# Performance work log

Measured on AMD Instinct MI355X. Metric: run time of the kernel, lower is better.

Reference implementation:

```python
import jax, jax.numpy as jnp
import numpy as np


def _bilinear_sample(img, x_s, y_s):
    # img: [B,H,W,C], x_s/y_s: [B,H,W] normalized coords in [-1,1]
    B, H, W, C = img.shape
    # map [-1,1] -> pixel coords [0, W-1] / [0, H-1]
    x = 0.5 * (x_s + 1.0) * (W - 1)
    y = 0.5 * (y_s + 1.0) * (H - 1)

    x0 = jnp.floor(x).astype(jnp.int32)
    x1 = x0 + 1
    y0 = jnp.floor(y).astype(jnp.int32)
    y1 = y0 + 1

    x0c = jnp.clip(x0, 0, W - 1)
    x1c = jnp.clip(x1, 0, W - 1)
    y0c = jnp.clip(y0, 0, H - 1)
    y1c = jnp.clip(y1, 0, H - 1)

    b = jnp.arange(B, dtype=jnp.int32)[:, None, None]  # [B,1,1] broadcast over H,W
    Ia = img[b, y0c, x0c]  # [B,H,W,C] top-left
    Ib = img[b, y1c, x0c]  # bottom-left
    Ic = img[b, y0c, x1c]  # top-right
    Id = img[b, y1c, x1c]  # bottom-right

    x0f = x0c.astype(img.dtype)
    x1f = x1c.astype(img.dtype)
    y0f = y0c.astype(img.dtype)
    y1f = y1c.astype(img.dtype)

    wa = ((x1f - x) * (y1f - y))[..., None]
    wb = ((x1f - x) * (y - y0f))[..., None]
    wc = ((x - x0f) * (y1f - y))[..., None]
    wd = ((x - x0f) * (y - y0f))[..., None]

    return wa * Ia + wb * Ib + wc * Ic + wd * Id


def setup_inputs() -> dict:
    key = jax.random.key(0)
    k1, k2, k3 = jax.random.split(key, 3)
    B, H, W, C = 16, 256, 256, 32
    batch_inputs = jax.random.normal(k1, (B, H, W, C), dtype=jnp.float32)
    x_s = jax.random.uniform(k2, (B, H, W), dtype=jnp.float32, minval=-1.0, maxval=1.0)
    y_s = jax.random.uniform(k3, (B, H, W), dtype=jnp.float32, minval=-1.0, maxval=1.0)
    return {"batch_inputs": batch_inputs, "x_s": x_s, "y_s": y_s}


def reference(batch_inputs, x_s, y_s):
    return _bilinear_sample(batch_inputs, x_s, y_s)
```

## Files before the change

kernel.cpp:

```cpp
#include <hip/hip_runtime.h>


constexpr int Bn = 16;
constexpr int Hn = 256;
constexpr int Wn = 256;
constexpr int Cn = 32;
constexpr int CG = Cn / 4;
constexpr int NP = 4;

typedef float f4 __attribute__((ext_vector_type(4)));

__global__ __launch_bounds__(256) void bilinear_kernel(
    const float* __restrict__ img,
    const float* __restrict__ xs,
    const float* __restrict__ ys,
    float* __restrict__ out)
{
    const int tid = threadIdx.x;
    const int cg  = tid & 7;
    const int lp  = tid >> 3;
    const int base_pix = blockIdx.x * 128 + lp;

    int pix[NP];
    float xsv[NP], ysv[NP];
#pragma unroll
    for (int g = 0; g < NP; ++g) {
        pix[g] = base_pix + g * 32;
        xsv[g] = __builtin_nontemporal_load(xs + pix[g]);
        ysv[g] = __builtin_nontemporal_load(ys + pix[g]);
    }

    float wa[NP], wb[NP], wc[NP], wd[NP];
    const f4* pa[NP];
    const f4* pb[NP];
    const f4* pc[NP];
    const f4* pd[NP];

#pragma unroll
    for (int g = 0; g < NP; ++g) {
        const float x = 0.5f * (xsv[g] + 1.0f) * (float)(Wn - 1);
        const float y = 0.5f * (ysv[g] + 1.0f) * (float)(Hn - 1);

        const int x0 = (int)floorf(x);
        const int y0 = (int)floorf(y);

        const int x0c = min(max(x0, 0), Wn - 1);
        const int x1c = min(max(x0 + 1, 0), Wn - 1);
        const int y0c = min(max(y0, 0), Hn - 1);
        const int y1c = min(max(y0 + 1, 0), Hn - 1);

        const float wx1 = (float)x1c - x;
        const float wx0 = x - (float)x0c;
        const float wy1 = (float)y1c - y;
        const float wy0 = y - (float)y0c;

        wa[g] = wx1 * wy1;
        wb[g] = wx1 * wy0;
        wc[g] = wx0 * wy1;
        wd[g] = wx0 * wy0;

        const int b = pix[g] >> 16;
        const size_t imgbase = (size_t)b * (size_t)(Hn * Wn * Cn);

        pa[g] = (const f4*)(img + imgbase + ((size_t)(y0c * Wn + x0c)) * Cn) + cg;
        pb[g] = (const f4*)(img + imgbase + ((size_t)(y1c * Wn + x0c)) * Cn) + cg;
        pc[g] = (const f4*)(img + imgbase + ((size_t)(y0c * Wn + x1c)) * Cn) + cg;
        pd[g] = (const f4*)(img + imgbase + ((size_t)(y1c * Wn + x1c)) * Cn) + cg;
    }

    f4 va[NP], vb[NP], vc[NP], vd[NP];
#pragma unroll
    for (int g = 0; g < NP; ++g) {
        va[g] = *pa[g];
        vb[g] = *pb[g];
        vc[g] = *pc[g];
        vd[g] = *pd[g];
    }

#pragma unroll
    for (int g = 0; g < NP; ++g) {
        f4 o;
        o.x = wa[g] * va[g].x + wb[g] * vb[g].x + wc[g] * vc[g].x + wd[g] * vd[g].x;
        o.y = wa[g] * va[g].y + wb[g] * vb[g].y + wc[g] * vc[g].y + wd[g] * vd[g].y;
        o.z = wa[g] * va[g].z + wb[g] * vb[g].z + wc[g] * vc[g].z + wd[g] * vd[g].z;
        o.w = wa[g] * va[g].w + wb[g] * vb[g].w + wc[g] * vc[g].w + wd[g] * vd[g].w;

        f4* op = (f4*)out + (size_t)pix[g] * CG + cg;
        __builtin_nontemporal_store(o, op);
    }
}

extern "C" void kernel_launch(void* const* d_in, const int* in_sizes, int n_in,
                              void* d_out, int out_size, void* d_ws, size_t ws_size,
                              hipStream_t stream)
{
    const float* img = (const float*)d_in[0];
    const float* xs  = (const float*)d_in[1];
    const float* ys  = (const float*)d_in[2];
    float* out       = (float*)d_out;

    const int total_pixels = Bn * Hn * Wn;
    const int block = 256;
    const int grid  = total_pixels / 128;

    bilinear_kernel<<<grid, block, 0, stream>>>(img, xs, ys, out);
}
```

Before: 250.0 us.

## Bin samples by image tile and gather from LDS tiles

Replaces the direct random-gather kernel with a four-stage pipeline. A histogram kernel counts sample pixels per 16x16 source tile, a scan turns the counts into offsets, and a scatter kernel writes pixel ids and coordinates into bins. A gather kernel then loads each 17x17x32 tile into shared memory and interpolates from it. The aim is to replace scattered global-memory gathers with one coalesced tile load per block. The costs are extra kernel launches, contended atomics, workspace traffic and output stores in random order. The old kernel stays as a fallback when the workspace is too small.

```diff
diff --git a/kernel.cpp b/kernel.cpp
--- a/kernel.cpp
+++ b/kernel.cpp
@@ -6,9 +6,171 @@
 constexpr int Wn = 256;
 constexpr int Cn = 32;
 constexpr int CG = Cn / 4;
+constexpr int NPIX = Bn * Hn * Wn;
+constexpr int TS = 16;
+constexpr int TH = TS + 1;
+constexpr int NB = Bn * (Hn / TS) * (Wn / TS);
+
+typedef float f4 __attribute__((ext_vector_type(4)));
+
+constexpr size_t WS_CNT  = 0;
+constexpr size_t WS_OFF  = 16 * 1024;
+constexpr size_t WS_CUR  = 32 * 1024;
+constexpr size_t WS_IDS  = 48 * 1024;
+constexpr size_t WS_XY   = WS_IDS + (size_t)NPIX * 4;
+constexpr size_t WS_NEED = WS_XY + (size_t)NPIX * 8;
+
+__global__ __launch_bounds__(256) void hist_k(
+    const float* __restrict__ xs, const float* __restrict__ ys,
+    unsigned* __restrict__ cnt)
+{
+    const int i = (blockIdx.x * 256 + threadIdx.x) * 4;
+    const f4 xv = *(const f4*)(xs + i);
+    const f4 yv = *(const f4*)(ys + i);
+    const int b = i >> 16;
+#pragma unroll
+    for (int j = 0; j < 4; ++j) {
+        const float x = 0.5f * (xv[j] + 1.0f) * (float)(Wn - 1);
+        const float y = 0.5f * (yv[j] + 1.0f) * (float)(Hn - 1);
+        int x0 = (int)floorf(x);
+        int y0 = (int)floorf(y);
+        x0 = min(max(x0, 0), Wn - 1);
+        y0 = min(max(y0, 0), Hn - 1);
+        const int bin = (b << 8) + ((y0 >> 4) << 4) + (x0 >> 4);
+        atomicAdd(&cnt[bin], 1u);
+    }
+}
+
+__global__ __launch_bounds__(1024) void scan_k(
+    const unsigned* __restrict__ cnt,
+    unsigned* __restrict__ off, unsigned* __restrict__ cur)
+{
+    __shared__ unsigned sc[1024];
+    const int t = threadIdx.x;
+    const uint4 c = ((const uint4*)cnt)[t];
+    const unsigned s = c.x + c.y + c.z + c.w;
+    sc[t] = s;
+    __syncthreads();
+    for (int d = 1; d < 1024; d <<= 1) {
+        const unsigned v = (t >= d) ? sc[t - d] : 0u;
+        __syncthreads();
+        sc[t] += v;
+        __syncthreads();
+    }
+    const unsigned excl = sc[t] - s;
+    uint4 o;
+    o.x = excl;
+    o.y = o.x + c.x;
+    o.z = o.y + c.y;
+    o.w = o.z + c.z;
+    ((uint4*)off)[t] = o;
+    ((uint4*)cur)[t] = o;
+}
+
+__global__ __launch_bounds__(256) void scat_k(
+    const float* __restrict__ xs, const float* __restrict__ ys,
+    unsigned* __restrict__ cur, unsigned* __restrict__ ids,
+    float2* __restrict__ xy)
+{
+    const int i = (blockIdx.x * 256 + threadIdx.x) * 4;
+    const f4 xv = *(const f4*)(xs + i);
+    const f4 yv = *(const f4*)(ys + i);
+    const int b = i >> 16;
+#pragma unroll
+    for (int j = 0; j < 4; ++j) {
+        const float x = 0.5f * (xv[j] + 1.0f) * (float)(Wn - 1);
+        const float y = 0.5f * (yv[j] + 1.0f) * (float)(Hn - 1);
+        int x0 = (int)floorf(x);
+        int y0 = (int)floorf(y);
+        x0 = min(max(x0, 0), Wn - 1);
+        y0 = min(max(y0, 0), Hn - 1);
+        const int bin = (b << 8) + ((y0 >> 4) << 4) + (x0 >> 4);
+        const unsigned pos = atomicAdd(&cur[bin], 1u);
+        ids[pos] = (unsigned)(i + j);
+        xy[pos] = make_float2(xv[j], yv[j]);
+    }
+}
+
+__global__ __launch_bounds__(256) void gather_k(
+    const float* __restrict__ img,
+    const unsigned* __restrict__ cnt, const unsigned* __restrict__ off,
+    const unsigned* __restrict__ ids, const float2* __restrict__ xy,
+    float* __restrict__ out)
+{
+    const int bin = blockIdx.x;
+    const unsigned npix = cnt[bin];
+    if (npix == 0u) return;
+    const unsigned base = off[bin];
+    const int b  = bin >> 8;
+    const int ty = (bin >> 4) & 15;
+    const int tx = bin & 15;
+
+    __shared__ float tile[TH * TH * Cn];
+
+    const float* imgb = img + (size_t)b * (size_t)(Hn * Wn * Cn);
+    const int tid = threadIdx.x;
+
+    for (int k = tid; k < TH * TH * (Cn / 4); k += 256) {
+        const int r = k / (TH * (Cn / 4));
+        const int m = k - r * (TH * (Cn / 4));
+        const int c = m >> 3;
+        const int q = m & 7;
+        const int gy = min(ty * TS + r, Hn - 1);
+        const int gx = min(tx * TS + c, Wn - 1);
+        const f4 v = *(const f4*)(imgb + ((size_t)(gy * Wn + gx)) * Cn + q * 4);
+        *(f4*)&tile[(r * TH + c) * Cn + q * 4] = v;
+    }
+    __syncthreads();
+
+    const int slot = tid >> 3;
+    const int cg   = tid & 7;
+
+    for (unsigned i = slot; i < npix; i += 32) {
+        const unsigned pos = base + i;
+        const unsigned pix = ids[pos];
+        const float2 cxy = xy[pos];
+
+        const float x = 0.5f * (cxy.x + 1.0f) * (float)(Wn - 1);
+        const float y = 0.5f * (cxy.y + 1.0f) * (float)(Hn - 1);
+        const int x0 = (int)floorf(x);
+        const int y0 = (int)floorf(y);
+        const int x0c = min(max(x0, 0), Wn - 1);
+        const int x1c = min(x0 + 1, Wn - 1);
+        const int y0c = min(max(y0, 0), Hn - 1);
+        const int y1c = min(y0 + 1, Hn - 1);
+
+        const float wx1 = (float)x1c - x;
+        const float wx0 = x - (float)x0c;
+        const float wy1 = (float)y1c - y;
+        const float wy0 = y - (float)y0c;
+
+        const float wa = wx1 * wy1;
+        const float wb = wx1 * wy0;
+        const float wc = wx0 * wy1;
+        const float wd = wx0 * wy0;
+
+        const int lx0 = x0c - tx * TS;
+        const int lx1 = x1c - tx * TS;
+        const int ly0 = y0c - ty * TS;
+        const int ly1 = y1c - ty * TS;
+
+        const f4 va = *(const f4*)&tile[(ly0 * TH + lx0) * Cn + cg * 4];
+        const f4 vb = *(const f4*)&tile[(ly1 * TH + lx0) * Cn + cg * 4];
+        const f4 vc = *(const f4*)&tile[(ly0 * TH + lx1) * Cn + cg * 4];
+        const f4 vd = *(const f4*)&tile[(ly1 * TH + lx1) * Cn + cg * 4];
+
+        f4 o;
+        o.x = wa * va.x + wb * vb.x + wc * vc.x + wd * vd.x;
+        o.y = wa * va.y + wb * vb.y + wc * vc.y + wd * vd.y;
+        o.z = wa * va.z + wb * vb.z + wc * vc.z + wd * vd.z;
+        o.w = wa * va.w + wb * vb.w + wc * vc.w + wd * vd.w;
+
+        f4* op = (f4*)out + (size_t)pix * CG + cg;
+        __builtin_nontemporal_store(o, op);
+    }
+}
+
 constexpr int NP = 4;
-
-typedef float f4 __attribute__((ext_vector_type(4)));
 
 __global__ __launch_bounds__(256) void bilinear_kernel(
     const float* __restrict__ img,
@@ -40,28 +202,22 @@
     for (int g = 0; g < NP; ++g) {
         const float x = 0.5f * (xsv[g] + 1.0f) * (float)(Wn - 1);
         const float y = 0.5f * (ysv[g] + 1.0f) * (float)(Hn - 1);
-
         const int x0 = (int)floorf(x);
         const int y0 = (int)floorf(y);
-
         const int x0c = min(max(x0, 0), Wn - 1);
         const int x1c = min(max(x0 + 1, 0), Wn - 1);
         const int y0c = min(max(y0, 0), Hn - 1);
         const int y1c = min(max(y0 + 1, 0), Hn - 1);
-
         const float wx1 = (float)x1c - x;
         const float wx0 = x - (float)x0c;
         const float wy1 = (float)y1c - y;
         const float wy0 = y - (float)y0c;
-
         wa[g] = wx1 * wy1;
         wb[g] = wx1 * wy0;
         wc[g] = wx0 * wy1;
         wd[g] = wx0 * wy0;
-
         const int b = pix[g] >> 16;
         const size_t imgbase = (size_t)b * (size_t)(Hn * Wn * Cn);
-
         pa[g] = (const f4*)(img + imgbase + ((size_t)(y0c * Wn + x0c)) * Cn) + cg;
         pb[g] = (const f4*)(img + imgbase + ((size_t)(y1c * Wn + x0c)) * Cn) + cg;
         pc[g] = (const f4*)(img + imgbase + ((size_t)(y0c * Wn + x1c)) * Cn) + cg;
@@ -84,7 +240,6 @@
         o.y = wa[g] * va[g].y + wb[g] * vb[g].y + wc[g] * vc[g].y + wd[g] * vd[g].y;
         o.z = wa[g] * va[g].z + wb[g] * vb[g].z + wc[g] * vc[g].z + wd[g] * vd[g].z;
         o.w = wa[g] * va[g].w + wb[g] * vb[g].w + wc[g] * vc[g].w + wd[g] * vd[g].w;
-
         f4* op = (f4*)out + (size_t)pix[g] * CG + cg;
         __builtin_nontemporal_store(o, op);
     }
@@ -99,9 +254,23 @@
     const float* ys  = (const float*)d_in[2];
     float* out       = (float*)d_out;
 
-    const int total_pixels = Bn * Hn * Wn;
-    const int block = 256;
-    const int grid  = total_pixels / 128;
-
-    bilinear_kernel<<<grid, block, 0, stream>>>(img, xs, ys, out);
-}
+    if (ws_size < WS_NEED || d_ws == nullptr) {
+        bilinear_kernel<<<NPIX / 128, 256, 0, stream>>>(img, xs, ys, out);
+        return;
+    }
+
+    char* ws = (char*)d_ws;
+    unsigned* cnt = (unsigned*)(ws + WS_CNT);
+    unsigned* off = (unsigned*)(ws + WS_OFF);
+    unsigned* cur = (unsigned*)(ws + WS_CUR);
+    unsigned* ids = (unsigned*)(ws + WS_IDS);
+    float2*   xy  = (float2*)(ws + WS_XY);
+
+    hipMemsetAsync(cnt, 0, NB * sizeof(unsigned), stream);
+
+    const int cblocks = NPIX / (256 * 4);
+    hist_k<<<cblocks, 256, 0, stream>>>(xs, ys, cnt);
+    scan_k<<<1, 1024, 0, stream>>>(cnt, off, cur);
+    scat_k<<<cblocks, 256, 0, stream>>>(xs, ys, cur, ids, xy);
+    gather_k<<<NB, 256, 0, stream>>>(img, cnt, off, ids, xy, out);
+}
```

Measured after the change: 374.5 us. +49.8%, slower.
